# Performance work log

Measured on AMD Instinct MI355X. Metric: run time of the kernel, lower is better.

Reference implementation:

```python
import jax, jax.numpy as jnp
import numpy as np

ADAPT_RATE = 0.05


def setup_inputs() -> dict:
    key = jax.random.key(0)
    k1, k2, k3 = jax.random.split(key, 3)
    B, T, DIN, DOUT = 64, 256, 1024, 1024
    x = jax.random.normal(k1, (B, T, DIN), dtype=jnp.float32)
    W = jax.random.normal(k2, (DOUT, DIN), dtype=jnp.float32) / np.sqrt(DIN)
    b = jax.random.normal(k3, (DOUT,), dtype=jnp.float32) * 0.01
    threshold = jnp.ones((DOUT,), dtype=jnp.float32)
    return {"x": x, "W": W, "b": b, "threshold": threshold}


def reference(x, W, b, threshold):
    # Precompute the per-timestep linear once as a single big GEMM: [B,T,O]
    pre = jnp.einsum('bti,oi->bto', x, W) + b
    B, T, O = pre.shape

    def step(carry, pre_t):
        mem, thr = carry
        mem = mem + pre_t                       # membrane accumulate [B,O]
        s = (mem >= thr).astype(pre_t.dtype)    # hard threshold spike
        # adaptive threshold: in-place .data update in torch (no grad path)
        thr = thr + ADAPT_RATE * (s.mean(axis=0) - 0.5)
        mem = mem * (1.0 - s)                   # reset where spiked
        return (mem, thr), s

    mem0 = jnp.zeros((B, O), dtype=x.dtype)
    (_, _), spikes = jax.lax.scan(step, (mem0, threshold), jnp.swapaxes(pre, 0, 1))
    return jnp.swapaxes(spikes, 0, 1)  # [B,T,O]
```

## Files before the change

### kernel.cpp

```cpp
#include <hip/hip_runtime.h>

#define B_ 64
#define T_ 256
#define DIN_ 1024
#define DOUT_ 1024

typedef int v4i  __attribute__((ext_vector_type(4)));
typedef int v16i __attribute__((ext_vector_type(16)));

#define PRE_BYTES 134217728ULL
#define XS_BYTES  83886080ULL
#define WSL_BYTES 5242880ULL
#define SPM_BYTES 2097152ULL

__global__ __launch_bounds__(256) void snn_split_x(
    const float* __restrict__ x, char* __restrict__ xs)
{
    const int W    = blockIdx.x * 4 + (threadIdx.x >> 6);
    const int lane = threadIdx.x & 63;
    const int mt = W & 1, kt = (W >> 1) & 31, t0 = W >> 6;
    const int m = lane & 31, kh = lane >> 5;
    const int b = mt * 32 + m;

    const float* src = x + ((size_t)b * T_ + t0) * DIN_ + kt * 32 + kh * 16;
    float f[16];
    *(float4*)(f)      = *(const float4*)(src);
    *(float4*)(f + 4)  = *(const float4*)(src + 4);
    *(float4*)(f + 8)  = *(const float4*)(src + 8);
    *(float4*)(f + 12) = *(const float4*)(src + 12);

    unsigned pk[5][4];
#pragma unroll
    for (int s = 0; s < 5; ++s)
        pk[s][0] = pk[s][1] = pk[s][2] = pk[s][3] = 0u;
#pragma unroll
    for (int j = 0; j < 16; ++j) {
        float v = f[j] * 0.125f;
#pragma unroll
        for (int s = 0; s < 5; ++s) {
            const float ml = (s == 0) ? 64.f : 128.f;
            const float sv = __builtin_rintf(v * ml);
            v = v * ml - sv;
            const int iv = (int)sv;
            pk[s][j >> 2] |= ((unsigned)iv & 0xffu) << ((j & 3) * 8);
        }
    }
#pragma unroll
    for (int s = 0; s < 5; ++s) {
        char* dst = xs + (size_t)(((s * 256 + t0) * 32 + kt) * 2 + mt) * 1024
                       + lane * 16;
        *(uint4*)dst = make_uint4(pk[s][0], pk[s][1], pk[s][2], pk[s][3]);
    }
}

__global__ __launch_bounds__(256) void snn_split_w(
    const float* __restrict__ Wt, char* __restrict__ wsl)
{
    const int W    = blockIdx.x * 4 + (threadIdx.x >> 6);
    const int lane = threadIdx.x & 63;
    const int kt = W & 31, ot = W >> 5;
    const int n = lane & 31, kh = lane >> 5;
    const int o = ot * 32 + n;

    const float* src = Wt + (size_t)o * DIN_ + kt * 32 + kh * 16;
    float f[16];
    *(float4*)(f)      = *(const float4*)(src);
    *(float4*)(f + 4)  = *(const float4*)(src + 4);
    *(float4*)(f + 8)  = *(const float4*)(src + 8);
    *(float4*)(f + 12) = *(const float4*)(src + 12);

    unsigned pk[5][4];
#pragma unroll
    for (int s = 0; s < 5; ++s)
        pk[s][0] = pk[s][1] = pk[s][2] = pk[s][3] = 0u;
#pragma unroll
    for (int j = 0; j < 16; ++j) {
        float v = f[j] * 4.0f;
#pragma unroll
        for (int s = 0; s < 5; ++s) {
            const float ml = (s == 0) ? 64.f : 128.f;
            const float sv = __builtin_rintf(v * ml);
            v = v * ml - sv;
            const int iv = (int)sv;
            pk[s][j >> 2] |= ((unsigned)iv & 0xffu) << ((j & 3) * 8);
        }
    }
#pragma unroll
    for (int s = 0; s < 5; ++s) {
        char* dst = wsl + (size_t)((s * 32 + ot) * 32 + kt) * 1024 + lane * 16;
        *(uint4*)dst = make_uint4(pk[s][0], pk[s][1], pk[s][2], pk[s][3]);
    }
}

__global__ __launch_bounds__(256, 2) void snn_gemm_i8(
    const char* __restrict__ xs, const char* __restrict__ wsl,
    const float* __restrict__ bias, double* __restrict__ pre)
{
    const int t0 = blockIdx.x >> 3;
    const int oB = blockIdx.x & 7;
    const int tid = threadIdx.x;
    const int lane = tid & 63;
    const int ws = __builtin_amdgcn_readfirstlane(tid >> 6);
    const int wm  = ws >> 1;
    const int wop = (ws & 1) * 2;
    const int lo  = lane * 16;

    v16i zero;
#pragma unroll
    for (int r = 0; r < 16; ++r) zero[r] = 0;
    v16i acc[2][5];
#pragma unroll
    for (int p = 0; p < 2; ++p)
#pragma unroll
        for (int g = 0; g < 5; ++g) acc[p][g] = zero;

    const char* ab  = xs  + (size_t)(t0 * 64 + wm) * 1024 + lo;
    const char* bb0 = wsl + (size_t)((oB * 4 + wop + 0) * 32) * 1024 + lo;
    const char* bb1 = wsl + (size_t)((oB * 4 + wop + 1) * 32) * 1024 + lo;

    for (int kt = 0; kt < 32; ++kt) {
        v4i a[5], b0[5], b1[5];
#pragma unroll
        for (int s = 0; s < 5; ++s)
            a[s]  = *(const v4i*)(ab  + (size_t)s * 16777216 + kt * 2048);
#pragma unroll
        for (int s = 0; s < 5; ++s)
            b0[s] = *(const v4i*)(bb0 + (size_t)s * 1048576 + kt * 1024);
#pragma unroll
        for (int s = 0; s < 5; ++s)
            b1[s] = *(const v4i*)(bb1 + (size_t)s * 1048576 + kt * 1024);

        __builtin_amdgcn_s_setprio(1);
#pragma unroll
        for (int i = 0; i < 5; ++i) {
#pragma unroll
            for (int j = 0; j < 5 - i; ++j) {
                acc[0][i + j] = __builtin_amdgcn_mfma_i32_32x32x32_i8(
                    a[i], b0[j], acc[0][i + j], 0, 0, 0);
                acc[1][i + j] = __builtin_amdgcn_mfma_i32_32x32x32_i8(
                    a[i], b1[j], acc[1][i + j], 0, 0, 0);
            }
        }
        __builtin_amdgcn_s_setprio(0);
    }

    const int n = lane & 31, lh = lane >> 5;
#pragma unroll
    for (int o2 = 0; o2 < 2; ++o2) {
        const int o = oB * 128 + (wop + o2) * 32 + n;
        const double bv = (double)bias[o];
        double* dst = pre + ((size_t)t0 * DOUT_ + o) * 64 + wm * 32;
#pragma unroll
        for (int r = 0; r < 16; ++r) {
            const int row = (r & 3) + 8 * (r >> 2) + 4 * lh;
            double v = (double)acc[o2][4][r];
            v = v * 0.0078125 + (double)acc[o2][3][r];
            v = v * 0.0078125 + (double)acc[o2][2][r];
            v = v * 0.0078125 + (double)acc[o2][1][r];
            v = v * 0.0078125 + (double)acc[o2][0][r];
            dst[row] = v * 0x1p-11 + bv;
        }
    }
}

__global__ __launch_bounds__(256, 2) void snn_gemm_fb(
    const float* __restrict__ x, const float* __restrict__ W,
    const float* __restrict__ bias, double* __restrict__ pre)
{
    __shared__ float smem[2][8 * 72 + 8 * 256];
    const int t0 = blockIdx.x & 255;
    const int o0 = blockIdx.x >> 8;
    const int tid = threadIdx.x;
    const int to = tid & 31;
    const int tb = tid >> 5;

    double acc[8][8];
#pragma unroll
    for (int i = 0; i < 8; ++i)
#pragma unroll
        for (int j = 0; j < 8; ++j) acc[i][j] = 0.0;

    const int arow = tid >> 2;
    const int ak2  = (tid & 3) * 2;
    const float* xg = x + (size_t)(t0 + 256 * arow) * DIN_ + ak2;
    const float* wg = W + (size_t)(o0 * 256 + tid) * DIN_;

    float2 f2  = *(const float2*)(xg);
    float4 bq0 = *(const float4*)(wg);
    float4 bq1 = *(const float4*)(wg + 4);

    for (int kc = 0; kc < DIN_ / 8; ++kc) {
        float* base = smem[kc & 1];
        float (*AsF)[72]  = (float(*)[72])base;
        float (*BsF)[256] = (float(*)[256])(base + 8 * 72);
        AsF[ak2 + 0][arow] = f2.x;
        AsF[ak2 + 1][arow] = f2.y;
        BsF[0][tid] = bq0.x;  BsF[1][tid] = bq0.y;
        BsF[2][tid] = bq0.z;  BsF[3][tid] = bq0.w;
        BsF[4][tid] = bq1.x;  BsF[5][tid] = bq1.y;
        BsF[6][tid] = bq1.z;  BsF[7][tid] = bq1.w;
        __syncthreads();
        if (kc + 1 < DIN_ / 8) {
            f2  = *(const float2*)(xg + (kc + 1) * 8);
            bq0 = *(const float4*)(wg + (kc + 1) * 8);
            bq1 = *(const float4*)(wg + (kc + 1) * 8 + 4);
        }
#pragma unroll
        for (int k = 0; k < 8; ++k) {
            const float4 af0 = *(const float4*)&AsF[k][tb * 8];
            const float4 af1 = *(const float4*)&AsF[k][tb * 8 + 4];
            const float4 bf0 = *(const float4*)&BsF[k][to * 4];
            const float4 bf1 = *(const float4*)&BsF[k][128 + to * 4];
            double a[8], b[8];
            a[0] = (double)af0.x; a[1] = (double)af0.y;
            a[2] = (double)af0.z; a[3] = (double)af0.w;
            a[4] = (double)af1.x; a[5] = (double)af1.y;
            a[6] = (double)af1.z; a[7] = (double)af1.w;
            b[0] = (double)bf0.x; b[1] = (double)bf0.y;
            b[2] = (double)bf0.z; b[3] = (double)bf0.w;
            b[4] = (double)bf1.x; b[5] = (double)bf1.y;
            b[6] = (double)bf1.z; b[7] = (double)bf1.w;
#pragma unroll
            for (int i = 0; i < 8; ++i)
#pragma unroll
                for (int j = 0; j < 8; ++j)
                    acc[i][j] += a[i] * b[j];
        }
        __syncthreads();
    }

    double biasd[8];
#pragma unroll
    for (int j = 0; j < 8; ++j)
        biasd[j] = (double)bias[o0 * 256 + (j >> 2) * 128 + to * 4 + (j & 3)];
    double (*trans)[67] = (double(*)[67])smem[0];
    for (int c = 0; c < 16; ++c) {
        __syncthreads();
        const int j4  = c >> 3;
        const int tlo = (c & 7) * 4;
        if (to >= tlo && to < tlo + 4) {
#pragma unroll
            for (int p4 = 0; p4 < 4; ++p4) {
                const int r = (to - tlo) * 4 + p4;
                const int j = j4 * 4 + p4;
#pragma unroll
                for (int i = 0; i < 8; ++i)
                    trans[r][tb * 8 + i] = acc[i][j] + biasd[j];
            }
        }
        __syncthreads();
#pragma unroll
        for (int q = 0; q < 4; ++q) {
            const int idx = tid + 256 * q;
            const int b  = idx & 63;
            const int oc = idx >> 6;
            pre[(size_t)(t0 * DOUT_ + o0 * 256 + c * 16 + oc) * 64 + b] = trans[oc][b];
        }
    }
}

#define SCAN_LOAD(PV, TB)                                                      \
    do {                                                                       \
        _Pragma("unroll")                                                      \
        for (int j = 0; j < 16; ++j)                                           \
            PV[j] = p[(size_t)((TB) + j) * (DOUT_ * 64)];                      \
    } while (0)

#define SCAN_STEP(PV, TB)                                                      \
    do {                                                                       \
        _Pragma("unroll")                                                      \
        for (int j = 0; j < 16; ++j) {                                         \
            mem += PV[j];                                                      \
            const bool s = (mem >= thr);                                       \
            const unsigned long long msk = __ballot(s);                        \
            thr += 0.05 * ((double)__popcll(msk) * (1.0 / 64.0) - 0.5);        \
            if (spM) {                                                         \
                if (lane == 0) spM[(size_t)((TB) + j) * DOUT_ + o] = msk;      \
            } else {                                                           \
                outD[(size_t)lane * (T_ * DOUT_) +                             \
                     (size_t)((TB) + j) * DOUT_ + o] = s ? 1.0f : 0.0f;        \
            }                                                                  \
            mem = s ? 0.0 : mem;                                               \
        }                                                                      \
    } while (0)

__global__ __launch_bounds__(256) void snn_scan(
    const double* __restrict__ pre, const float* __restrict__ thr_in,
    unsigned long long* __restrict__ spM, float* __restrict__ outD)
{
    const int wid  = (blockIdx.x * blockDim.x + threadIdx.x) >> 6;
    const int lane = threadIdx.x & 63;
    if (wid >= DOUT_) return;
    const int o = wid;

    double mem = 0.0;
    double thr = (double)thr_in[o];
    const double* p = pre + (size_t)o * 64 + lane;

    double pvA[16], pvB[16];
    SCAN_LOAD(pvA, 0);
    for (int t = 0; t < T_; t += 32) {
        if (t + 16 < T_) SCAN_LOAD(pvB, t + 16);
        SCAN_STEP(pvA, t);
        if (t + 32 < T_) SCAN_LOAD(pvA, t + 32);
        SCAN_STEP(pvB, t + 16);
    }
}

__global__ __launch_bounds__(256) void snn_expand(
    const unsigned long long* __restrict__ spM, float* __restrict__ out)
{
    const int idx = blockIdx.x * 256 + threadIdx.x;
    const int og = idx & 255;
    const int t  = idx >> 8;
    const unsigned long long* mp = spM + (size_t)t * DOUT_ + og * 4;
    const unsigned long long m0 = mp[0], m1 = mp[1], m2 = mp[2], m3 = mp[3];
    float* op = out + (size_t)t * DOUT_ + og * 4;
#pragma unroll
    for (int b = 0; b < 64; ++b) {
        float4 v;
        v.x = (float)((m0 >> b) & 1ULL);
        v.y = (float)((m1 >> b) & 1ULL);
        v.z = (float)((m2 >> b) & 1ULL);
        v.w = (float)((m3 >> b) & 1ULL);
        *(float4*)(op + (size_t)b * (T_ * DOUT_)) = v;
    }
}

extern "C" void kernel_launch(void* const* d_in, const int* in_sizes, int n_in,
                              void* d_out, int out_size, void* d_ws, size_t ws_size,
                              hipStream_t stream) {
    const float* x    = (const float*)d_in[0];
    const float* W    = (const float*)d_in[1];
    const float* bias = (const float*)d_in[2];
    const float* thr  = (const float*)d_in[3];
    float* out = (float*)d_out;

    double* pre = (double*)d_ws;
    const size_t need = PRE_BYTES + XS_BYTES + WSL_BYTES + SPM_BYTES;

    if (ws_size >= need) {
        char* xs  = (char*)d_ws + PRE_BYTES;
        char* wsl = xs + XS_BYTES;
        unsigned long long* spM = (unsigned long long*)(wsl + WSL_BYTES);
        snn_split_x<<<4096, 256, 0, stream>>>(x, xs);
        snn_split_w<<<256, 256, 0, stream>>>(W, wsl);
        snn_gemm_i8<<<2048, 256, 0, stream>>>(xs, wsl, bias, pre);
        snn_scan<<<256, 256, 0, stream>>>(pre, thr, spM, nullptr);
        snn_expand<<<256, 256, 0, stream>>>(spM, out);
    } else {
        const bool two_stage = (ws_size >= PRE_BYTES + SPM_BYTES);
        unsigned long long* spM =
            two_stage ? (unsigned long long*)((char*)d_ws + PRE_BYTES) : nullptr;
        snn_gemm_fb<<<1024, 256, 0, stream>>>(x, W, bias, pre);
        snn_scan<<<256, 256, 0, stream>>>(pre, thr, spM, two_stage ? nullptr : out);
        if (two_stage)
            snn_expand<<<256, 256, 0, stream>>>(spM, out);
    }
}
```

Baseline: 419.8 us.

## Stage W slices through double-buffered LDS with async loads and prefetch A

The int8-split GEMM now covers a 64-wide output chunk per block instead of 128, doubling the grid, and each wave accumulates one output tile rather than two. Two waves fill a double-buffered LDS stage with W slices via global_load_lds, and all waves read B from LDS. A slices are prefetched one k-step ahead into registers. This trades halved register pressure (allowing 3 blocks per SIMD set) and overlapped loads for an extra barrier per k-step and more A-tile reloads across the larger grid.

Measured after the change: 437.0 us. +4.1%, slower.

```diff
diff --git a/kernel.cpp b/kernel.cpp
--- a/kernel.cpp
+++ b/kernel.cpp
@@ -12,6 +12,12 @@
 #define XS_BYTES  83886080ULL
 #define WSL_BYTES 5242880ULL
 #define SPM_BYTES 2097152ULL
+
+__device__ __forceinline__ void async_copy16(const void* g, void* l) {
+    __builtin_amdgcn_global_load_lds(
+        (const __attribute__((address_space(1))) void*)g,
+        (__attribute__((address_space(3))) void*)l, 16, 0, 0);
+}
 
 __global__ __launch_bounds__(256) void snn_split_x(
     const float* __restrict__ x, char* __restrict__ xs)
@@ -92,74 +98,89 @@
     }
 }
 
-__global__ __launch_bounds__(256, 2) void snn_gemm_i8(
+__global__ __launch_bounds__(256, 3) void snn_gemm_i8(
     const char* __restrict__ xs, const char* __restrict__ wsl,
     const float* __restrict__ bias, double* __restrict__ pre)
 {
-    const int t0 = blockIdx.x >> 3;
-    const int oB = blockIdx.x & 7;
+    __shared__ __align__(16) char lds[2][10 * 1024];
+    const int t0 = blockIdx.x >> 4;
+    const int oc = blockIdx.x & 15;
     const int tid = threadIdx.x;
     const int lane = tid & 63;
     const int ws = __builtin_amdgcn_readfirstlane(tid >> 6);
-    const int wm  = ws >> 1;
-    const int wop = (ws & 1) * 2;
-    const int lo  = lane * 16;
-
-    v16i zero;
-#pragma unroll
-    for (int r = 0; r < 16; ++r) zero[r] = 0;
-    v16i acc[2][5];
-#pragma unroll
-    for (int p = 0; p < 2; ++p)
-#pragma unroll
-        for (int g = 0; g < 5; ++g) acc[p][g] = zero;
-
-    const char* ab  = xs  + (size_t)(t0 * 64 + wm) * 1024 + lo;
-    const char* bb0 = wsl + (size_t)((oB * 4 + wop + 0) * 32) * 1024 + lo;
-    const char* bb1 = wsl + (size_t)((oB * 4 + wop + 1) * 32) * 1024 + lo;
+    const int wm = ws >> 1;
+    const int wo = ws & 1;
+    const int lo = lane * 16;
+
+    v16i acc[5];
+#pragma unroll
+    for (int g = 0; g < 5; ++g)
+#pragma unroll
+        for (int r = 0; r < 16; ++r) acc[g][r] = 0;
+
+    const char* ab = xs + (size_t)(t0 * 64 + wm) * 1024 + lo;
+    const char* sg = wsl + (size_t)((oc * 2 + ws) * 32) * 1024 + lo;
+
+    v4i aC[5], aN[5];
+#pragma unroll
+    for (int s = 0; s < 5; ++s)
+        aC[s] = *(const v4i*)(ab + (size_t)s * 16777216);
+    if (ws < 2) {
+#pragma unroll
+        for (int s = 0; s < 5; ++s)
+            async_copy16(sg + (size_t)s * 1048576, &lds[0][(ws * 5 + s) * 1024]);
+    }
+    __syncthreads();
 
     for (int kt = 0; kt < 32; ++kt) {
-        v4i a[5], b0[5], b1[5];
+        if (kt + 1 < 32) {
+            const size_t ko = (size_t)(kt + 1);
+#pragma unroll
+            for (int s = 0; s < 5; ++s)
+                aN[s] = *(const v4i*)(ab + (size_t)s * 16777216 + ko * 2048);
+            if (ws < 2) {
+                char* buf = lds[(kt + 1) & 1];
+#pragma unroll
+                for (int s = 0; s < 5; ++s)
+                    async_copy16(sg + (size_t)s * 1048576 + ko * 1024,
+                                 &buf[(ws * 5 + s) * 1024]);
+            }
+        }
+        const char* cbuf = lds[kt & 1];
+        v4i b[5];
 #pragma unroll
         for (int s = 0; s < 5; ++s)
-            a[s]  = *(const v4i*)(ab  + (size_t)s * 16777216 + kt * 2048);
-#pragma unroll
-        for (int s = 0; s < 5; ++s)
-            b0[s] = *(const v4i*)(bb0 + (size_t)s * 1048576 + kt * 1024);
-#pragma unroll
-        for (int s = 0; s < 5; ++s)
-            b1[s] = *(const v4i*)(bb1 + (size_t)s * 1048576 + kt * 1024);
+            b[s] = *(const v4i*)(cbuf + (wo * 5 + s) * 1024 + lo);
 
         __builtin_amdgcn_s_setprio(1);
 #pragma unroll
         for (int i = 0; i < 5; ++i) {
 #pragma unroll
-            for (int j = 0; j < 5 - i; ++j) {
-                acc[0][i + j] = __builtin_amdgcn_mfma_i32_32x32x32_i8(
-                    a[i], b0[j], acc[0][i + j], 0, 0, 0);
-                acc[1][i + j] = __builtin_amdgcn_mfma_i32_32x32x32_i8(
-                    a[i], b1[j], acc[1][i + j], 0, 0, 0);
-            }
+            for (int j = 0; j < 5 - i; ++j)
+                acc[i + j] = __builtin_amdgcn_mfma_i32_32x32x32_i8(
+                    aC[i], b[j], acc[i + j], 0, 0, 0);
         }
         __builtin_amdgcn_s_setprio(0);
+        __syncthreads();
+        if (kt + 1 < 32) {
+#pragma unroll
+            for (int s = 0; s < 5; ++s) aC[s] = aN[s];
+        }
     }
 
     const int n = lane & 31, lh = lane >> 5;
-#pragma unroll
-    for (int o2 = 0; o2 < 2; ++o2) {
-        const int o = oB * 128 + (wop + o2) * 32 + n;
-        const double bv = (double)bias[o];
-        double* dst = pre + ((size_t)t0 * DOUT_ + o) * 64 + wm * 32;
-#pragma unroll
-        for (int r = 0; r < 16; ++r) {
-            const int row = (r & 3) + 8 * (r >> 2) + 4 * lh;
-            double v = (double)acc[o2][4][r];
-            v = v * 0.0078125 + (double)acc[o2][3][r];
-            v = v * 0.0078125 + (double)acc[o2][2][r];
-            v = v * 0.0078125 + (double)acc[o2][1][r];
-            v = v * 0.0078125 + (double)acc[o2][0][r];
-            dst[row] = v * 0x1p-11 + bv;
-        }
+    const int o = oc * 64 + wo * 32 + n;
+    const double bv = (double)bias[o];
+    double* dst = pre + ((size_t)t0 * DOUT_ + o) * 64 + wm * 32;
+#pragma unroll
+    for (int r = 0; r < 16; ++r) {
+        const int row = (r & 3) + 8 * (r >> 2) + 4 * lh;
+        double v = (double)acc[4][r];
+        v = v * 0.0078125 + (double)acc[3][r];
+        v = v * 0.0078125 + (double)acc[2][r];
+        v = v * 0.0078125 + (double)acc[1][r];
+        v = v * 0.0078125 + (double)acc[0][r];
+        dst[row] = v * 0x1p-11 + bv;
     }
 }
 
@@ -345,7 +366,7 @@
         unsigned long long* spM = (unsigned long long*)(wsl + WSL_BYTES);
         snn_split_x<<<4096, 256, 0, stream>>>(x, xs);
         snn_split_w<<<256, 256, 0, stream>>>(W, wsl);
-        snn_gemm_i8<<<2048, 256, 0, stream>>>(xs, wsl, bias, pre);
+        snn_gemm_i8<<<4096, 256, 0, stream>>>(xs, wsl, bias, pre);
         snn_scan<<<256, 256, 0, stream>>>(pre, thr, spM, nullptr);
         snn_expand<<<256, 256, 0, stream>>>(spM, out);
     } else {
```

## Stage int8 GEMM operands through LDS with triple-buffered async loads

Applied to the files above, without the earlier changes.

The int8 split GEMM now uses 512-thread blocks that each cover two timesteps instead of one. Operand slices are staged into LDS with global_load_lds async copies, triple-buffered with a two-iteration prefetch distance. The A and B tiles are shared across waves in place of redundant per-wave global loads. This is meant to cut global/L2 traffic and hide load latency behind the MFMAs, at the cost of 120KB of LDS per block (which may limit occupancy) and a barrier every k-step. The fallback path's expand grid size also changes, but that path does not run by default.

New measurement: 391.4 us. -6.8%, faster.

```diff
diff --git a/kernel.cpp b/kernel.cpp
--- a/kernel.cpp
+++ b/kernel.cpp
@@ -12,6 +12,12 @@
 #define XS_BYTES  83886080ULL
 #define WSL_BYTES 5242880ULL
 #define SPM_BYTES 2097152ULL
+
+__device__ __forceinline__ void async_copy16(const void* g, void* l) {
+    __builtin_amdgcn_global_load_lds(
+        (const __attribute__((address_space(1))) void*)g,
+        (__attribute__((address_space(3))) void*)l, 16, 0, 0);
+}
 
 __global__ __launch_bounds__(256) void snn_split_x(
     const float* __restrict__ x, char* __restrict__ xs)
@@ -92,64 +98,100 @@
     }
 }
 
-__global__ __launch_bounds__(256, 2) void snn_gemm_i8(
+__global__ __launch_bounds__(512, 2) void snn_gemm_i8(
     const char* __restrict__ xs, const char* __restrict__ wsl,
     const float* __restrict__ bias, double* __restrict__ pre)
 {
-    const int t0 = blockIdx.x >> 3;
-    const int oB = blockIdx.x & 7;
+    __shared__ __align__(16) char ldsA[3][20 * 1024];
+    __shared__ __align__(16) char ldsB[3][20 * 1024];
+    const int tp = blockIdx.x >> 3;
+    const int oc = blockIdx.x & 7;
     const int tid = threadIdx.x;
     const int lane = tid & 63;
     const int ws = __builtin_amdgcn_readfirstlane(tid >> 6);
-    const int wm  = ws >> 1;
-    const int wop = (ws & 1) * 2;
+    const int wm  = ws & 3;
+    const int wog = ws >> 2;
     const int lo  = lane * 16;
 
-    v16i zero;
-#pragma unroll
-    for (int r = 0; r < 16; ++r) zero[r] = 0;
     v16i acc[2][5];
 #pragma unroll
     for (int p = 0; p < 2; ++p)
 #pragma unroll
-        for (int g = 0; g < 5; ++g) acc[p][g] = zero;
-
-    const char* ab  = xs  + (size_t)(t0 * 64 + wm) * 1024 + lo;
-    const char* bb0 = wsl + (size_t)((oB * 4 + wop + 0) * 32) * 1024 + lo;
-    const char* bb1 = wsl + (size_t)((oB * 4 + wop + 1) * 32) * 1024 + lo;
-
+        for (int g = 0; g < 5; ++g)
+#pragma unroll
+            for (int r = 0; r < 16; ++r) acc[p][g][r] = 0;
+
+    const char* sgA = xs + ((size_t)(2 * tp + (ws >> 1)) * 65536
+                            + (size_t)(ws & 1) * 1024) + lo;
+    const char* sgB = wsl + (size_t)(oc * 4 + (ws - 4)) * 32768 + lo;
+
+#define STAGE_BATCH(JB, BUF)                                                   \
+    do {                                                                       \
+        if (ws < 4) {                                                          \
+            _Pragma("unroll")                                                  \
+            for (int s = 0; s < 5; ++s)                                        \
+                async_copy16(sgA + (size_t)s * 16777216 + (size_t)(JB) * 2048, \
+                             &ldsA[BUF][(ws * 5 + s) * 1024]);                 \
+        } else {                                                               \
+            _Pragma("unroll")                                                  \
+            for (int s = 0; s < 5; ++s)                                        \
+                async_copy16(sgB + (size_t)s * 1048576 + (size_t)(JB) * 1024,  \
+                             &ldsB[BUF][((ws - 4) * 5 + s) * 1024]);           \
+        }                                                                      \
+    } while (0)
+
+    STAGE_BATCH(0, 0);
+    STAGE_BATCH(1, 1);
+
+    int rd = 0, st = 2;
     for (int kt = 0; kt < 32; ++kt) {
+        if (kt < 31) asm volatile("s_waitcnt vmcnt(5)" ::: "memory");
+        else         asm volatile("s_waitcnt vmcnt(0)" ::: "memory");
+        __builtin_amdgcn_s_barrier();
+        asm volatile("" ::: "memory");
+
+        if (kt + 2 < 32) STAGE_BATCH(kt + 2, st);
+
+        const char* bufA = ldsA[rd];
+        const char* bufB = ldsB[rd];
         v4i a[5], b0[5], b1[5];
 #pragma unroll
-        for (int s = 0; s < 5; ++s)
-            a[s]  = *(const v4i*)(ab  + (size_t)s * 16777216 + kt * 2048);
-#pragma unroll
-        for (int s = 0; s < 5; ++s)
-            b0[s] = *(const v4i*)(bb0 + (size_t)s * 1048576 + kt * 1024);
-#pragma unroll
-        for (int s = 0; s < 5; ++s)
-            b1[s] = *(const v4i*)(bb1 + (size_t)s * 1048576 + kt * 1024);
+        for (int s = 0; s < 5; ++s) {
+            a[s]  = *(const v4i*)(bufA + (wm * 5 + s) * 1024 + lo);
+            b0[s] = *(const v4i*)(bufB + ((wog * 2 + 0) * 5 + s) * 1024 + lo);
+            b1[s] = *(const v4i*)(bufB + ((wog * 2 + 1) * 5 + s) * 1024 + lo);
+        }
 
         __builtin_amdgcn_s_setprio(1);
 #pragma unroll
         for (int i = 0; i < 5; ++i) {
 #pragma unroll
-            for (int j = 0; j < 5 - i; ++j) {
+            for (int j = 0; j < 5 - i; ++j)
                 acc[0][i + j] = __builtin_amdgcn_mfma_i32_32x32x32_i8(
                     a[i], b0[j], acc[0][i + j], 0, 0, 0);
+        }
+#pragma unroll
+        for (int i = 0; i < 5; ++i) {
+#pragma unroll
+            for (int j = 0; j < 5 - i; ++j)
                 acc[1][i + j] = __builtin_amdgcn_mfma_i32_32x32x32_i8(
                     a[i], b1[j], acc[1][i + j], 0, 0, 0);
-            }
         }
         __builtin_amdgcn_s_setprio(0);
-    }
+
+        rd = (rd == 2) ? 0 : rd + 1;
+        st = (st == 2) ? 0 : st + 1;
+    }
+#undef STAGE_BATCH
 
     const int n = lane & 31, lh = lane >> 5;
+    const int tout = 2 * tp + (wm >> 1);
+    const int boff = (wm & 1) * 32;
 #pragma unroll
     for (int o2 = 0; o2 < 2; ++o2) {
-        const int o = oB * 128 + (wop + o2) * 32 + n;
+        const int o = oc * 128 + (wog * 2 + o2) * 32 + n;
         const double bv = (double)bias[o];
-        double* dst = pre + ((size_t)t0 * DOUT_ + o) * 64 + wm * 32;
+        double* dst = pre + ((size_t)tout * DOUT_ + o) * 64 + boff;
 #pragma unroll
         for (int r = 0; r < 16; ++r) {
             const int row = (r & 3) + 8 * (r >> 2) + 4 * lh;
@@ -345,7 +387,7 @@
         unsigned long long* spM = (unsigned long long*)(wsl + WSL_BYTES);
         snn_split_x<<<4096, 256, 0, stream>>>(x, xs);
         snn_split_w<<<256, 256, 0, stream>>>(W, wsl);
-        snn_gemm_i8<<<2048, 256, 0, stream>>>(xs, wsl, bias, pre);
+        snn_gemm_i8<<<1024, 512, 0, stream>>>(xs, wsl, bias, pre);
         snn_scan<<<256, 256, 0, stream>>>(pre, thr, spM, nullptr);
         snn_expand<<<256, 256, 0, stream>>>(spM, out);
     } else {
@@ -355,6 +397,6 @@
         snn_gemm_fb<<<1024, 256, 0, stream>>>(x, W, bias, pre);
         snn_scan<<<256, 256, 0, stream>>>(pre, thr, spM, two_stage ? nullptr : out);
         if (two_stage)
-            snn_expand<<<256, 256, 0, stream>>>(spM, out);
-    }
-}
+            snn_expand<<<1024, 256, 0, stream>>>(spM, out);
+    }
+}
```
